# Kernel optimization log

Measured on AMD Instinct MI355X. Metric: run time of the kernel, lower is better.

The kernel has to match this reference:

```python
import jax, jax.numpy as jnp
import numpy as np

N = 100000   # nodes
E = 1600000  # edges (avg degree 16)
D = 32       # feature dim

def setup_inputs() -> dict:
    key = jax.random.key(0)
    k1, k2, k3, k4 = jax.random.split(key, 4)
    feat = jax.random.normal(k1, (N, D), dtype=jnp.float32)
    e_feat = jax.random.normal(k2, (E, 1), dtype=jnp.float32)
    src = jax.random.randint(k3, (E,), 0, N)
    dst = jax.random.randint(k4, (E,), 0, N)
    return {"feat": feat, "e_feat": e_feat, "src": src, "dst": dst}

def reference(feat, e_feat, src, dst):
    n = feat.shape[0]
    ones = jnp.ones(src.shape[0], dtype=feat.dtype)
    # degrees computed on the full graph (before self-loop removal), as in DGL code
    out_deg = jax.ops.segment_sum(ones, src, num_segments=n)
    in_deg = jax.ops.segment_sum(ones, dst, num_segments=n)
    src_norm = jnp.power(jnp.clip(out_deg, 1.0, None), -0.5)[:, None]  # [N,1]
    dst_norm = jnp.power(jnp.clip(in_deg, 1.0, None), -0.5)[:, None]   # [N,1]
    # remove_self_loop: mask out self-loop edges in the aggregation only
    mask = (src != dst).astype(feat.dtype)[:, None]                    # [E,1]
    # u_mul_e: gather normalized src features, multiply by edge weight
    msg = (feat * src_norm)[src] * (e_feat * mask)                     # [E,D]
    agg = jax.ops.segment_sum(msg, dst, num_segments=n)                # [N,D]
    out = feat - agg * dst_norm
    return jnp.sum(jnp.abs(out), axis=1)                               # [N]
```

## Files before the change

### kernel.cpp

```cpp
#include <hip/hip_runtime.h>

#define D 32
#define RANGE 128
#define RMAX 800
#define JC 512
#define SCAN_CHUNK 4096
#define CAP 2560

__global__ __launch_bounds__(512) void count_kernel(
        const int* __restrict__ src, const int* __restrict__ dst,
        int* __restrict__ cnt, int E, int R, int chunk) {
    __shared__ int cd[RMAX];
    __shared__ int cs[RMAX];
    int j = blockIdx.x;
    for (int i = threadIdx.x; i < R; i += blockDim.x) { cd[i] = 0; cs[i] = 0; }
    __syncthreads();
    int e0 = j * chunk, e1 = min(E, e0 + chunk);
    for (int e = e0 + 2 * threadIdx.x; e < e1; e += 2 * blockDim.x) {
        if (e + 1 < e1) {
            int2 s2 = *(const int2*)(src + e);
            int2 d2 = *(const int2*)(dst + e);
            atomicAdd(&cd[d2.x >> 7], 1);
            atomicAdd(&cd[d2.y >> 7], 1);
            atomicAdd(&cs[s2.x >> 7], 1);
            atomicAdd(&cs[s2.y >> 7], 1);
        } else {
            atomicAdd(&cd[dst[e] >> 7], 1);
            atomicAdd(&cs[src[e] >> 7], 1);
        }
    }
    __syncthreads();
    for (int i = threadIdx.x; i < R; i += blockDim.x) {
        cnt[(size_t)i * JC + j]       = cd[i];
        cnt[(size_t)(R + i) * JC + j] = cs[i];
    }
}

__global__ void scan_part(const int* __restrict__ deg, int* __restrict__ offsets,
                          int* __restrict__ blockSums, int n) {
    __shared__ int lds[256];
    int t = threadIdx.x;
    int base = blockIdx.x * SCAN_CHUNK + t * 16;
    int v[16];
    int tsum = 0;
#pragma unroll
    for (int i = 0; i < 16; i++) {
        int idx = base + i;
        int x = (idx < n) ? deg[idx] : 0;
        v[i] = tsum;
        tsum += x;
    }
    lds[t] = tsum;
    __syncthreads();
    for (int off = 1; off < 256; off <<= 1) {
        int val = (t >= off) ? lds[t - off] : 0;
        __syncthreads();
        lds[t] += val;
        __syncthreads();
    }
    int texcl = (t == 0) ? 0 : lds[t - 1];
    if (t == 255) blockSums[blockIdx.x] = lds[255];
#pragma unroll
    for (int i = 0; i < 16; i++) {
        int idx = base + i;
        if (idx < n) offsets[idx] = texcl + v[i];
    }
}

__global__ void scan_top(int* __restrict__ blockSums, int nb) {
    __shared__ int lds[256];
    int t = threadIdx.x;
    lds[t] = (t < nb) ? blockSums[t] : 0;
    __syncthreads();
    for (int off = 1; off < 256; off <<= 1) {
        int val = (t >= off) ? lds[t - off] : 0;
        __syncthreads();
        lds[t] += val;
        __syncthreads();
    }
    if (t < nb) blockSums[t] = (t == 0) ? 0 : lds[t - 1];
}

__global__ void scan_add(int* __restrict__ offsets, const int* __restrict__ blockSums, int n) {
    int i = blockIdx.x * blockDim.x + threadIdx.x;
    if (i < n) offsets[i] += blockSums[i / SCAN_CHUNK];
}

__global__ __launch_bounds__(512) void reorder_kernel(
        const int* __restrict__ src, const int* __restrict__ dst,
        const float* __restrict__ ef, const int* __restrict__ offs,
        unsigned int* __restrict__ recsS_m, uint2* __restrict__ recs,
        int E, int R, int chunk) {
    __shared__ int curD[RMAX];
    __shared__ int curS[RMAX];
    int j = blockIdx.x;
    for (int i = threadIdx.x; i < R; i += blockDim.x) {
        curD[i] = offs[(size_t)i * JC + j];
        curS[i] = offs[(size_t)(R + i) * JC + j];
    }
    __syncthreads();
    int e0 = j * chunk, e1 = min(E, e0 + chunk);
    for (int e = e0 + 2 * threadIdx.x; e < e1; e += 2 * blockDim.x) {
        if (e + 1 < e1) {
            int2 s2 = *(const int2*)(src + e);
            int2 d2 = *(const int2*)(dst + e);
            float2 w2 = *(const float2*)(ef + e);
            int ps0 = atomicAdd(&curS[s2.x >> 7], 1);
            int ps1 = atomicAdd(&curS[s2.y >> 7], 1);
            recsS_m[ps0] = (unsigned)s2.x;
            recsS_m[ps1] = (unsigned)s2.y;
            float w0 = (s2.x == d2.x) ? 0.0f : w2.x;
            float w1 = (s2.y == d2.y) ? 0.0f : w2.y;
            int pd0 = atomicAdd(&curD[d2.x >> 7], 1);
            int pd1 = atomicAdd(&curD[d2.y >> 7], 1);
            recs[pd0] = make_uint2((unsigned)s2.x | ((unsigned)(d2.x & (RANGE - 1)) << 17),
                                   __float_as_uint(w0));
            recs[pd1] = make_uint2((unsigned)s2.y | ((unsigned)(d2.y & (RANGE - 1)) << 17),
                                   __float_as_uint(w1));
        } else {
            int s = src[e], d = dst[e];
            int ps = atomicAdd(&curS[s >> 7], 1);
            recsS_m[ps] = (unsigned)s;
            float w = (s == d) ? 0.0f : ef[e];
            int pd = atomicAdd(&curD[d >> 7], 1);
            recs[pd] = make_uint2((unsigned)s | ((unsigned)(d & (RANGE - 1)) << 17),
                                  __float_as_uint(w));
        }
    }
}

__device__ __forceinline__ unsigned short f2bf(float x) {
    unsigned u = __float_as_uint(x);
    u += 0x7FFFu + ((u >> 16) & 1u);
    return (unsigned short)(u >> 16);
}

__global__ void srcnorm_convert(const unsigned int* __restrict__ recsS_m,
                                const int* __restrict__ offs, const float* __restrict__ feat,
                                unsigned short* __restrict__ featb, int E, int n, int R) {
    __shared__ int cnt[RANGE];
    int r = blockIdx.x;
    int base = r * RANGE;
    int lim = min(n - base, RANGE);
    for (int i = threadIdx.x; i < RANGE; i += blockDim.x) cnt[i] = 0;
    __syncthreads();
    int start = offs[(size_t)(R + r) * JC];
    int end = (r + 1 < R) ? offs[(size_t)(R + r + 1) * JC] : 2 * E;
    for (int i = start + threadIdx.x; i < end; i += blockDim.x)
        atomicAdd(&cnt[recsS_m[i] - base], 1);
    __syncthreads();
    int total4 = lim * 8;
    for (int i = threadIdx.x; i < total4; i += blockDim.x) {
        int row = i >> 3;
        float sn = rsqrtf((float)max(cnt[row], 1));
        float4 f = ((const float4*)(feat + (size_t)(base + row) * D))[i & 7];
        ushort4 u;
        u.x = f2bf(f.x * sn); u.y = f2bf(f.y * sn);
        u.z = f2bf(f.z * sn); u.w = f2bf(f.w * sn);
        ((ushort4*)(featb + (size_t)(base + row) * D))[i & 7] = u;
    }
}

__global__ __launch_bounds__(512) void gather_kernel(
        const float* __restrict__ feat, const unsigned short* __restrict__ featb,
        const uint2* __restrict__ recs, const int* __restrict__ offs,
        float* __restrict__ out, int E, int n, int R) {
    __shared__ uint2 srec[CAP];
    __shared__ int indeg[RANGE];
    __shared__ int pre[RANGE + 1];
    __shared__ int cur[RANGE];
    int r = blockIdx.x;
    int base = r * RANGE;
    int lim = min(n - base, RANGE);
    int start = offs[(size_t)r * JC];
    int end = (r + 1 < R) ? offs[(size_t)(r + 1) * JC] : E;
    int capEnd = min(end, start + CAP);
    for (int i = threadIdx.x; i < RANGE; i += blockDim.x) indeg[i] = 0;
    __syncthreads();
    for (int i = start + threadIdx.x; i < capEnd; i += blockDim.x)
        atomicAdd(&indeg[(recs[i].x >> 17) & 0x1FFu], 1);
    __syncthreads();
    if (threadIdx.x < RANGE) pre[threadIdx.x + 1] = indeg[threadIdx.x];
    if (threadIdx.x == 0) pre[0] = 0;
    __syncthreads();
    for (int off = 1; off < RANGE; off <<= 1) {
        int v = 0;
        if (threadIdx.x < RANGE) {
            int idx = threadIdx.x + 1;
            if (idx > off) v = pre[idx - off];
        }
        __syncthreads();
        if (threadIdx.x < RANGE) pre[threadIdx.x + 1] += v;
        __syncthreads();
    }
    if (threadIdx.x < RANGE) cur[threadIdx.x] = pre[threadIdx.x];
    __syncthreads();
    for (int i = start + threadIdx.x; i < capEnd; i += blockDim.x) {
        uint2 rec = recs[i];
        int dl = (rec.x >> 17) & 0x1FFu;
        int pos = atomicAdd(&cur[dl], 1);
        srec[pos] = make_uint2(rec.x & 0x1FFFFu, rec.y);
    }
    __syncthreads();
    int node = threadIdx.x >> 2;
    int c = threadIdx.x & 3;
    if (node >= lim) return;
    int p0i = pre[node];
    int cnt = pre[node + 1] - p0i;
    float a0 = 0.f, a1 = 0.f, a2 = 0.f, a3 = 0.f, a4 = 0.f, a5 = 0.f, a6 = 0.f, a7 = 0.f;
    int i = 0;
    for (; i + 2 <= cnt; i += 2) {
        uint2 q0 = srec[p0i + i];
        uint2 q1 = srec[p0i + i + 1];
        uint4 b0 = ((const uint4*)(featb + (size_t)q0.x * D))[c];
        uint4 b1 = ((const uint4*)(featb + (size_t)q1.x * D))[c];
        float w0 = __uint_as_float(q0.y);
        float w1 = __uint_as_float(q1.y);
        a0 += __uint_as_float(b0.x << 16) * w0 + __uint_as_float(b1.x << 16) * w1;
        a1 += __uint_as_float(b0.x & 0xFFFF0000u) * w0 + __uint_as_float(b1.x & 0xFFFF0000u) * w1;
        a2 += __uint_as_float(b0.y << 16) * w0 + __uint_as_float(b1.y << 16) * w1;
        a3 += __uint_as_float(b0.y & 0xFFFF0000u) * w0 + __uint_as_float(b1.y & 0xFFFF0000u) * w1;
        a4 += __uint_as_float(b0.z << 16) * w0 + __uint_as_float(b1.z << 16) * w1;
        a5 += __uint_as_float(b0.z & 0xFFFF0000u) * w0 + __uint_as_float(b1.z & 0xFFFF0000u) * w1;
        a6 += __uint_as_float(b0.w << 16) * w0 + __uint_as_float(b1.w << 16) * w1;
        a7 += __uint_as_float(b0.w & 0xFFFF0000u) * w0 + __uint_as_float(b1.w & 0xFFFF0000u) * w1;
    }
    if (i < cnt) {
        uint2 q = srec[p0i + i];
        uint4 b = ((const uint4*)(featb + (size_t)q.x * D))[c];
        float w = __uint_as_float(q.y);
        a0 += __uint_as_float(b.x << 16) * w;
        a1 += __uint_as_float(b.x & 0xFFFF0000u) * w;
        a2 += __uint_as_float(b.y << 16) * w;
        a3 += __uint_as_float(b.y & 0xFFFF0000u) * w;
        a4 += __uint_as_float(b.z << 16) * w;
        a5 += __uint_as_float(b.z & 0xFFFF0000u) * w;
        a6 += __uint_as_float(b.w << 16) * w;
        a7 += __uint_as_float(b.w & 0xFFFF0000u) * w;
    }
    if (end - start > CAP) {
        for (int k = start + CAP; k < end; k++) {
            uint2 rec = recs[k];
            int dl = (rec.x >> 17) & 0x1FFu;
            if (dl == node) {
                cnt++;
                uint4 b = ((const uint4*)(featb + (size_t)(rec.x & 0x1FFFFu) * D))[c];
                float w = __uint_as_float(rec.y);
                a0 += __uint_as_float(b.x << 16) * w;
                a1 += __uint_as_float(b.x & 0xFFFF0000u) * w;
                a2 += __uint_as_float(b.y << 16) * w;
                a3 += __uint_as_float(b.y & 0xFFFF0000u) * w;
                a4 += __uint_as_float(b.z << 16) * w;
                a5 += __uint_as_float(b.z & 0xFFFF0000u) * w;
                a6 += __uint_as_float(b.w << 16) * w;
                a7 += __uint_as_float(b.w & 0xFFFF0000u) * w;
            }
        }
    }
    float dn = rsqrtf((float)max(cnt, 1));
    const float4* fr = (const float4*)(feat + (size_t)(base + node) * D);
    float4 fA = fr[c * 2];
    float4 fB = fr[c * 2 + 1];
    float v = fabsf(fA.x - a0 * dn) + fabsf(fA.y - a1 * dn) +
              fabsf(fA.z - a2 * dn) + fabsf(fA.w - a3 * dn) +
              fabsf(fB.x - a4 * dn) + fabsf(fB.y - a5 * dn) +
              fabsf(fB.z - a6 * dn) + fabsf(fB.w - a7 * dn);
    v += __shfl_xor(v, 1, 4);
    v += __shfl_xor(v, 2, 4);
    if (c == 0) out[base + node] = v;
}

extern "C" void kernel_launch(void* const* d_in, const int* in_sizes, int n_in,
                              void* d_out, int out_size, void* d_ws, size_t ws_size,
                              hipStream_t stream) {
    const float* feat   = (const float*)d_in[0];
    const float* e_feat = (const float*)d_in[1];
    const int*   src    = (const int*)d_in[2];
    const int*   dst    = (const int*)d_in[3];
    const int E = in_sizes[2];
    const int n = in_sizes[0] / D;
    float* out = (float*)d_out;

    const int R = (n + RANGE - 1) / RANGE;
    const int chunk = (((E + JC - 1) / JC) + 1) & ~1;
    const int total = 2 * R * JC;

    char* p = (char*)d_ws;
    int* cnt       = (int*)p;   p += ((size_t)total * 4 + 15) & ~(size_t)15;
    int* offs      = (int*)p;   p += ((size_t)total * 4 + 15) & ~(size_t)15;
    int* blockSums = (int*)p;   p += 256 * 4;
    uint2* recs    = (uint2*)p; p += ((size_t)E * 8 + 15) & ~(size_t)15;
    unsigned int* recsS = (unsigned int*)p; p += ((size_t)E * 4 + 15) & ~(size_t)15;
    unsigned short* featb = (unsigned short*)p;
    unsigned int* recsS_m = recsS - (size_t)E;

    count_kernel<<<JC, 512, 0, stream>>>(src, dst, cnt, E, R, chunk);

    int nb = (total + SCAN_CHUNK - 1) / SCAN_CHUNK;
    scan_part<<<nb, 256, 0, stream>>>(cnt, offs, blockSums, total);
    scan_top<<<1, 256, 0, stream>>>(blockSums, nb);
    scan_add<<<(total + 255) / 256, 256, 0, stream>>>(offs, blockSums, total);

    reorder_kernel<<<JC, 512, 0, stream>>>(src, dst, e_feat, offs, recsS_m, recs, E, R, chunk);

    srcnorm_convert<<<R, 256, 0, stream>>>(recsS_m, offs, feat, featb, E, n, R);

    gather_kernel<<<R, 512, 0, stream>>>(feat, featb, recs, offs, out, E, n, R);
}
```

Measured before the change: 164.0 us.

## Pad per-block bucket segments to aligned boundaries and raise gather LDS capacity

```diff
diff --git a/kernel.cpp b/kernel.cpp
--- a/kernel.cpp
+++ b/kernel.cpp
@@ -5,7 +5,9 @@
 #define RMAX 800
 #define JC 512
 #define SCAN_CHUNK 4096
-#define CAP 2560
+#define CAP 4096
+#define PAD_D 4
+#define PAD_S 8
 
 __global__ __launch_bounds__(512) void count_kernel(
         const int* __restrict__ src, const int* __restrict__ dst,
@@ -31,9 +33,10 @@
     }
     __syncthreads();
     for (int i = threadIdx.x; i < R; i += blockDim.x) {
-        cnt[(size_t)i * JC + j]       = cd[i];
-        cnt[(size_t)(R + i) * JC + j] = cs[i];
-    }
+        cnt[(size_t)i * JC + j]       = (cd[i] + (PAD_D - 1)) & ~(PAD_D - 1);
+        cnt[(size_t)(R + i) * JC + j] = (cs[i] + (PAD_S - 1)) & ~(PAD_S - 1);
+    }
+    if (j == 0 && threadIdx.x == 0) cnt[(size_t)2 * R * JC] = 0;
 }
 
 __global__ void scan_part(const int* __restrict__ deg, int* __restrict__ offsets,
@@ -89,14 +92,15 @@
 __global__ __launch_bounds__(512) void reorder_kernel(
         const int* __restrict__ src, const int* __restrict__ dst,
         const float* __restrict__ ef, const int* __restrict__ offs,
-        unsigned int* __restrict__ recsS_m, uint2* __restrict__ recs,
+        unsigned int* __restrict__ recsS, uint2* __restrict__ recs,
         int E, int R, int chunk) {
     __shared__ int curD[RMAX];
     __shared__ int curS[RMAX];
     int j = blockIdx.x;
+    int srcBase = offs[(size_t)R * JC];
     for (int i = threadIdx.x; i < R; i += blockDim.x) {
         curD[i] = offs[(size_t)i * JC + j];
-        curS[i] = offs[(size_t)(R + i) * JC + j];
+        curS[i] = offs[(size_t)(R + i) * JC + j] - srcBase;
     }
     __syncthreads();
     int e0 = j * chunk, e1 = min(E, e0 + chunk);
@@ -107,8 +111,8 @@
             float2 w2 = *(const float2*)(ef + e);
             int ps0 = atomicAdd(&curS[s2.x >> 7], 1);
             int ps1 = atomicAdd(&curS[s2.y >> 7], 1);
-            recsS_m[ps0] = (unsigned)s2.x;
-            recsS_m[ps1] = (unsigned)s2.y;
+            recsS[ps0] = (unsigned)s2.x;
+            recsS[ps1] = (unsigned)s2.y;
             float w0 = (s2.x == d2.x) ? 0.0f : w2.x;
             float w1 = (s2.y == d2.y) ? 0.0f : w2.y;
             int pd0 = atomicAdd(&curD[d2.x >> 7], 1);
@@ -120,13 +124,24 @@
         } else {
             int s = src[e], d = dst[e];
             int ps = atomicAdd(&curS[s >> 7], 1);
-            recsS_m[ps] = (unsigned)s;
+            recsS[ps] = (unsigned)s;
             float w = (s == d) ? 0.0f : ef[e];
             int pd = atomicAdd(&curD[d >> 7], 1);
             recs[pd] = make_uint2((unsigned)s | ((unsigned)(d & (RANGE - 1)) << 17),
                                   __float_as_uint(w));
         }
     }
+    __syncthreads();
+    for (int i = threadIdx.x; i < R; i += blockDim.x) {
+        int initD = offs[(size_t)i * JC + j];
+        int finD = curD[i];
+        int endD = initD + ((finD - initD + (PAD_D - 1)) & ~(PAD_D - 1));
+        for (int k = finD; k < endD; k++) recs[k] = make_uint2(511u << 17, 0u);
+        int initS = offs[(size_t)(R + i) * JC + j] - srcBase;
+        int finS = curS[i];
+        int endS = initS + ((finS - initS + (PAD_S - 1)) & ~(PAD_S - 1));
+        for (int k = finS; k < endS; k++) recsS[k] = 0xFFFFFFFFu;
+    }
 }
 
 __device__ __forceinline__ unsigned short f2bf(float x) {
@@ -135,7 +150,7 @@
     return (unsigned short)(u >> 16);
 }
 
-__global__ void srcnorm_convert(const unsigned int* __restrict__ recsS_m,
+__global__ void srcnorm_convert(const unsigned int* __restrict__ recsS,
                                 const int* __restrict__ offs, const float* __restrict__ feat,
                                 unsigned short* __restrict__ featb, int E, int n, int R) {
     __shared__ int cnt[RANGE];
@@ -144,10 +159,14 @@
     int lim = min(n - base, RANGE);
     for (int i = threadIdx.x; i < RANGE; i += blockDim.x) cnt[i] = 0;
     __syncthreads();
-    int start = offs[(size_t)(R + r) * JC];
-    int end = (r + 1 < R) ? offs[(size_t)(R + r + 1) * JC] : 2 * E;
-    for (int i = start + threadIdx.x; i < end; i += blockDim.x)
-        atomicAdd(&cnt[recsS_m[i] - base], 1);
+    int srcBase = offs[(size_t)R * JC];
+    int start = offs[(size_t)(R + r) * JC] - srcBase;
+    int end = ((r + 1 < R) ? offs[(size_t)(R + r + 1) * JC]
+                           : offs[(size_t)2 * R * JC]) - srcBase;
+    for (int i = start + threadIdx.x; i < end; i += blockDim.x) {
+        unsigned idx = recsS[i] - (unsigned)base;
+        if (idx < (unsigned)lim) atomicAdd(&cnt[idx], 1);
+    }
     __syncthreads();
     int total4 = lim * 8;
     for (int i = threadIdx.x; i < total4; i += blockDim.x) {
@@ -173,12 +192,14 @@
     int base = r * RANGE;
     int lim = min(n - base, RANGE);
     int start = offs[(size_t)r * JC];
-    int end = (r + 1 < R) ? offs[(size_t)(r + 1) * JC] : E;
-    int capEnd = min(end, start + CAP);
+    int end = (r + 1 < R) ? offs[(size_t)(r + 1) * JC] : offs[(size_t)R * JC];
     for (int i = threadIdx.x; i < RANGE; i += blockDim.x) indeg[i] = 0;
     __syncthreads();
-    for (int i = start + threadIdx.x; i < capEnd; i += blockDim.x)
-        atomicAdd(&indeg[(recs[i].x >> 17) & 0x1FFu], 1);
+    int placed0 = 0;
+    for (int i = start + threadIdx.x; i < end; i += blockDim.x) {
+        unsigned dl = recs[i].x >> 17;
+        if (dl < RANGE) { atomicAdd(&indeg[dl], 1); placed0++; }
+    }
     __syncthreads();
     if (threadIdx.x < RANGE) pre[threadIdx.x + 1] = indeg[threadIdx.x];
     if (threadIdx.x == 0) pre[0] = 0;
@@ -195,11 +216,16 @@
     }
     if (threadIdx.x < RANGE) cur[threadIdx.x] = pre[threadIdx.x];
     __syncthreads();
-    for (int i = start + threadIdx.x; i < capEnd; i += blockDim.x) {
-        uint2 rec = recs[i];
-        int dl = (rec.x >> 17) & 0x1FFu;
-        int pos = atomicAdd(&cur[dl], 1);
-        srec[pos] = make_uint2(rec.x & 0x1FFFFu, rec.y);
+    bool ovf = pre[RANGE] > CAP;
+    if (!ovf) {
+        for (int i = start + threadIdx.x; i < end; i += blockDim.x) {
+            uint2 rec = recs[i];
+            unsigned dl = rec.x >> 17;
+            if (dl < RANGE) {
+                int pos = atomicAdd(&cur[(int)dl], 1);
+                srec[pos] = make_uint2(rec.x & 0x1FFFFu, rec.y);
+            }
+        }
     }
     __syncthreads();
     int node = threadIdx.x >> 2;
@@ -208,42 +234,41 @@
     int p0i = pre[node];
     int cnt = pre[node + 1] - p0i;
     float a0 = 0.f, a1 = 0.f, a2 = 0.f, a3 = 0.f, a4 = 0.f, a5 = 0.f, a6 = 0.f, a7 = 0.f;
-    int i = 0;
-    for (; i + 2 <= cnt; i += 2) {
-        uint2 q0 = srec[p0i + i];
-        uint2 q1 = srec[p0i + i + 1];
-        uint4 b0 = ((const uint4*)(featb + (size_t)q0.x * D))[c];
-        uint4 b1 = ((const uint4*)(featb + (size_t)q1.x * D))[c];
-        float w0 = __uint_as_float(q0.y);
-        float w1 = __uint_as_float(q1.y);
-        a0 += __uint_as_float(b0.x << 16) * w0 + __uint_as_float(b1.x << 16) * w1;
-        a1 += __uint_as_float(b0.x & 0xFFFF0000u) * w0 + __uint_as_float(b1.x & 0xFFFF0000u) * w1;
-        a2 += __uint_as_float(b0.y << 16) * w0 + __uint_as_float(b1.y << 16) * w1;
-        a3 += __uint_as_float(b0.y & 0xFFFF0000u) * w0 + __uint_as_float(b1.y & 0xFFFF0000u) * w1;
-        a4 += __uint_as_float(b0.z << 16) * w0 + __uint_as_float(b1.z << 16) * w1;
-        a5 += __uint_as_float(b0.z & 0xFFFF0000u) * w0 + __uint_as_float(b1.z & 0xFFFF0000u) * w1;
-        a6 += __uint_as_float(b0.w << 16) * w0 + __uint_as_float(b1.w << 16) * w1;
-        a7 += __uint_as_float(b0.w & 0xFFFF0000u) * w0 + __uint_as_float(b1.w & 0xFFFF0000u) * w1;
-    }
-    if (i < cnt) {
-        uint2 q = srec[p0i + i];
-        uint4 b = ((const uint4*)(featb + (size_t)q.x * D))[c];
-        float w = __uint_as_float(q.y);
-        a0 += __uint_as_float(b.x << 16) * w;
-        a1 += __uint_as_float(b.x & 0xFFFF0000u) * w;
-        a2 += __uint_as_float(b.y << 16) * w;
-        a3 += __uint_as_float(b.y & 0xFFFF0000u) * w;
-        a4 += __uint_as_float(b.z << 16) * w;
-        a5 += __uint_as_float(b.z & 0xFFFF0000u) * w;
-        a6 += __uint_as_float(b.w << 16) * w;
-        a7 += __uint_as_float(b.w & 0xFFFF0000u) * w;
-    }
-    if (end - start > CAP) {
-        for (int k = start + CAP; k < end; k++) {
+    if (!ovf) {
+        int i = 0;
+        for (; i + 2 <= cnt; i += 2) {
+            uint2 q0 = srec[p0i + i];
+            uint2 q1 = srec[p0i + i + 1];
+            uint4 b0 = ((const uint4*)(featb + (size_t)q0.x * D))[c];
+            uint4 b1 = ((const uint4*)(featb + (size_t)q1.x * D))[c];
+            float w0 = __uint_as_float(q0.y);
+            float w1 = __uint_as_float(q1.y);
+            a0 += __uint_as_float(b0.x << 16) * w0 + __uint_as_float(b1.x << 16) * w1;
+            a1 += __uint_as_float(b0.x & 0xFFFF0000u) * w0 + __uint_as_float(b1.x & 0xFFFF0000u) * w1;
+            a2 += __uint_as_float(b0.y << 16) * w0 + __uint_as_float(b1.y << 16) * w1;
+            a3 += __uint_as_float(b0.y & 0xFFFF0000u) * w0 + __uint_as_float(b1.y & 0xFFFF0000u) * w1;
+            a4 += __uint_as_float(b0.z << 16) * w0 + __uint_as_float(b1.z << 16) * w1;
+            a5 += __uint_as_float(b0.z & 0xFFFF0000u) * w0 + __uint_as_float(b1.z & 0xFFFF0000u) * w1;
+            a6 += __uint_as_float(b0.w << 16) * w0 + __uint_as_float(b1.w << 16) * w1;
+            a7 += __uint_as_float(b0.w & 0xFFFF0000u) * w0 + __uint_as_float(b1.w & 0xFFFF0000u) * w1;
+        }
+        if (i < cnt) {
+            uint2 q = srec[p0i + i];
+            uint4 b = ((const uint4*)(featb + (size_t)q.x * D))[c];
+            float w = __uint_as_float(q.y);
+            a0 += __uint_as_float(b.x << 16) * w;
+            a1 += __uint_as_float(b.x & 0xFFFF0000u) * w;
+            a2 += __uint_as_float(b.y << 16) * w;
+            a3 += __uint_as_float(b.y & 0xFFFF0000u) * w;
+            a4 += __uint_as_float(b.z << 16) * w;
+            a5 += __uint_as_float(b.z & 0xFFFF0000u) * w;
+            a6 += __uint_as_float(b.w << 16) * w;
+            a7 += __uint_as_float(b.w & 0xFFFF0000u) * w;
+        }
+    } else {
+        for (int k = start; k < end; k++) {
             uint2 rec = recs[k];
-            int dl = (rec.x >> 17) & 0x1FFu;
-            if (dl == node) {
-                cnt++;
+            if ((rec.x >> 17) == (unsigned)node) {
                 uint4 b = ((const uint4*)(featb + (size_t)(rec.x & 0x1FFFFu) * D))[c];
                 float w = __uint_as_float(rec.y);
                 a0 += __uint_as_float(b.x << 16) * w;
@@ -283,16 +308,17 @@
 
     const int R = (n + RANGE - 1) / RANGE;
     const int chunk = (((E + JC - 1) / JC) + 1) & ~1;
-    const int total = 2 * R * JC;
-
+    const int total = 2 * R * JC + 1;
+
+    size_t recsCap  = (size_t)E + (size_t)(PAD_D - 1) * R * JC;
+    size_t recsSCap = (size_t)E + (size_t)(PAD_S - 1) * R * JC;
     char* p = (char*)d_ws;
-    int* cnt       = (int*)p;   p += ((size_t)total * 4 + 15) & ~(size_t)15;
-    int* offs      = (int*)p;   p += ((size_t)total * 4 + 15) & ~(size_t)15;
+    int* cnt       = (int*)p;   p += ((size_t)total * 4 + 31) & ~(size_t)31;
+    int* offs      = (int*)p;   p += ((size_t)total * 4 + 31) & ~(size_t)31;
     int* blockSums = (int*)p;   p += 256 * 4;
-    uint2* recs    = (uint2*)p; p += ((size_t)E * 8 + 15) & ~(size_t)15;
-    unsigned int* recsS = (unsigned int*)p; p += ((size_t)E * 4 + 15) & ~(size_t)15;
+    uint2* recs    = (uint2*)p; p += (recsCap * 8 + 31) & ~(size_t)31;
+    unsigned int* recsS = (unsigned int*)p; p += (recsSCap * 4 + 31) & ~(size_t)31;
     unsigned short* featb = (unsigned short*)p;
-    unsigned int* recsS_m = recsS - (size_t)E;
 
     count_kernel<<<JC, 512, 0, stream>>>(src, dst, cnt, E, R, chunk);
 
@@ -301,9 +327,9 @@
     scan_top<<<1, 256, 0, stream>>>(blockSums, nb);
     scan_add<<<(total + 255) / 256, 256, 0, stream>>>(offs, blockSums, total);
 
-    reorder_kernel<<<JC, 512, 0, stream>>>(src, dst, e_feat, offs, recsS_m, recs, E, R, chunk);
-
-    srcnorm_convert<<<R, 256, 0, stream>>>(recsS_m, offs, feat, featb, E, n, R);
+    reorder_kernel<<<JC, 512, 0, stream>>>(src, dst, e_feat, offs, recsS, recs, E, R, chunk);
+
+    srcnorm_convert<<<R, 256, 0, stream>>>(recsS, offs, feat, featb, E, n, R);
 
     gather_kernel<<<R, 512, 0, stream>>>(feat, featb, recs, offs, out, E, n, R);
 }
```

Result: slower. 181.5 us (+10.7%).
